# Optimization experiments

Measured on AMD Instinct MI355X. Metric: run time of the kernel, lower is better.

The kernel has to match this reference:

```python
import jax, jax.numpy as jnp
import numpy as np

N = 100000
E = 1600000
IN, HID, OUT = 512, 256, 32
K = 3
LAMBDA_AMP = 0.5


def setup_inputs() -> dict:
    key = jax.random.key(0)
    ks = jax.random.split(key, 6)
    x = jax.random.normal(ks[0], (N, IN), dtype=jnp.float32)
    edge_index = jax.random.randint(ks[1], (2, E), 0, N, dtype=jnp.int64)
    # MLP params (PyTorch Linear default init: U(-1/sqrt(fan_in), 1/sqrt(fan_in)))
    s1 = 1.0 / np.sqrt(IN)
    W1 = jax.random.uniform(ks[2], (IN, HID), jnp.float32, -s1, s1)
    b1 = jax.random.uniform(ks[3], (HID,), jnp.float32, -s1, s1)
    s2 = 1.0 / np.sqrt(HID)
    W2 = jax.random.uniform(ks[4], (HID, OUT), jnp.float32, -s2, s2)
    b2 = jax.random.uniform(ks[5], (OUT,), jnp.float32, -s2, s2)
    return {"x": x, "W1": W1, "b1": b1, "W2": W2, "b2": b2, "edge_index": edge_index}


def _gcn_norm(edge_index, n_nodes, dtype):
    # add self loops, symmetric normalization D^-1/2 (A+I) D^-1/2
    loop = jnp.arange(n_nodes, dtype=edge_index.dtype)
    row = jnp.concatenate([edge_index[0], loop])
    col = jnp.concatenate([edge_index[1], loop])
    w = jnp.ones(row.shape[0], dtype=dtype)
    deg = jax.ops.segment_sum(w, col, num_segments=n_nodes)
    dis = jnp.where(deg > 0, jax.lax.rsqrt(deg), 0.0)
    norm = dis[row] * w * dis[col]
    return row, col, norm


def _proximal_l21(x, lam):
    # row-wise soft-thresholding of L2 norms
    rn = jnp.sqrt(jnp.sum(x * x, axis=1))  # [N]
    safe = jnp.where(rn > 0, rn, 1.0)
    score = jnp.where(rn > 0, jnp.maximum(rn - lam, 0.0) / safe, 0.0)
    return score[:, None] * x


def reference(x, W1, b1, W2, b2, edge_index):
    # MLP (dropout inactive at inference)
    h = jax.nn.relu(x @ W1 + b1)
    h = h @ W2 + b2  # [N, OUT]

    row, col, norm = _gcn_norm(edge_index, N, h.dtype)

    lam = LAMBDA_AMP
    gamma = 1.0 / (2.0 * (1.0 - lam))
    hh = h
    xk = h
    for _ in range(K):
        # A_hat @ xk via gather-scale-scatter
        ax = jax.ops.segment_sum(norm[:, None] * xk[row], col, num_segments=N)
        lx = xk - ax  # L @ xk
        y = xk - gamma * 2.0 * (1.0 - lam) * lx
        xk = hh + _proximal_l21(y - hh, lam * gamma)
    return xk
```

## Files before the change

### kernel.cpp

```cpp
#include <hip/hip_runtime.h>
#include <cstdint>

#define NN 100000
#define EE 1600000
#define IN_F 512
#define HID_F 256
#define OUT_F 32
#define GSL 256
#define SLICE_W 12500
#define CAP 64

typedef float f32x4 __attribute__((ext_vector_type(4)));
typedef int   i32x4 __attribute__((ext_vector_type(4)));
typedef short s16x8 __attribute__((ext_vector_type(8)));
typedef uint32_t u32x4 __attribute__((ext_vector_type(4)));
typedef unsigned short u16;

static __device__ __forceinline__ u16 f2bf(float f) {
  uint32_t u = __builtin_bit_cast(uint32_t, f);
  u += 0x7FFFu + ((u >> 16) & 1u);
  return (u16)(u >> 16);
}

static __device__ __forceinline__ float bf2f(u16 v) {
  uint32_t u = ((uint32_t)v) << 16;
  return __builtin_bit_cast(float, u);
}

static __device__ __forceinline__ uint32_t pk_bf16(float a, float b) {
  uint32_t r;
  asm("v_cvt_pk_bf16_f32 %0, %1, %2" : "=v"(r) : "v"(a), "v"(b));
  return r;
}

__global__ __launch_bounds__(256) void k_prep(const float* __restrict__ w1,
                                              u16* __restrict__ w1f,
                                              const float* __restrict__ w2,
                                              u16* __restrict__ w2f,
                                              int* __restrict__ cur) {
  int b = blockIdx.x;
  int tid = threadIdx.x;
  if (b < 512) {
    int g = b * 256 + tid;
    int j    = g & 7;
    int lane = (g >> 3) & 63;
    int fnG  = (g >> 9) & 15;
    int kk   = g >> 13;
    int k = kk * 32 + (lane >> 4) * 8 + j;
    int n = fnG * 16 + (lane & 15);
    w1f[g] = f2bf(w1[k * HID_F + n]);
  } else if (b < 544) {
    int g = (b - 512) * 256 + tid;
    int j    = g & 7;
    int lane = (g >> 3) & 63;
    int ff   = g >> 9;
    int k = (ff >> 1) * 32 + (lane >> 4) * 8 + j;
    int n = (ff & 1) * 16 + (lane & 15);
    w2f[g] = f2bf(w2[k * OUT_F + n]);
  } else {
    int i = (b - 544) * 256 + tid;
    if (i < NN) cur[i] = 0;
  }
}

__global__ __launch_bounds__(256) void k_fillC(const int* __restrict__ row,
                                               const int* __restrict__ col,
                                               int* __restrict__ cur,
                                               int* __restrict__ csr) {
  const int slice = blockIdx.x & 7;
  const int g = blockIdx.x >> 3;
  const unsigned lo = (unsigned)slice * SLICE_W, hi = lo + SLICE_W;
  const i32x4* c4 = (const i32x4*)col;
  const i32x4* r4 = (const i32x4*)row;
  for (int i = g * 256 + threadIdx.x; i < EE / 4; i += GSL * 256) {
    i32x4 c = c4[i];
    i32x4 r = r4[i];
    #pragma unroll
    for (int k = 0; k < 4; ++k) {
      unsigned cc = (unsigned)c[k];
      if (cc >= lo && cc < hi) {
        int p = atomicAdd(&cur[cc], 1);
        if (p < CAP) csr[(int)cc * CAP + p] = r[k];
      }
    }
  }
}

__global__ __launch_bounds__(256, 4) void k_mlp(
    const float* __restrict__ x, const float* __restrict__ b1,
    const float* __restrict__ b2, const u16* __restrict__ w1f,
    const u16* __restrict__ w2f, const int* __restrict__ cnt,
    float* __restrict__ hout, u16* __restrict__ xs0) {
  __shared__ char smem[32768];
  char* aL  = smem;
  char* h1L = smem;

  const int tid  = threadIdx.x;
  const int lane = tid & 63;
  const int wid  = tid >> 6;
  const int wn   = wid;
  const int l16  = lane & 15;
  const int lq   = lane >> 4;
  const int row0 = blockIdx.x * 64;

  const f32x4 zf = {0.f, 0.f, 0.f, 0.f};
  f32x4 acc[4][4];
  #pragma unroll
  for (int i = 0; i < 4; ++i)
    #pragma unroll
    for (int j = 0; j < 4; ++j) acc[i][j] = zf;

  for (int kt = 0; kt < IN_F / 64; ++kt) {
    __syncthreads();
    #pragma unroll
    for (int p = 0; p < 4; ++p) {
      int v   = p * 256 + tid;
      int row = v >> 4;
      int f4  = v & 15;
      int grow = row0 + row;
      f32x4 xv = zf;
      if (grow < NN)
        xv = *(const f32x4*)(x + (size_t)grow * IN_F + kt * 64 + f4 * 4);
      uint32_t lo = pk_bf16(xv.x, xv.y);
      uint32_t hi = pk_bf16(xv.z, xv.w);
      uint64_t wv = (uint64_t)lo | ((uint64_t)hi << 32);
      int kb = (f4 * 8) ^ ((row & 7) << 4);
      *(uint64_t*)(aL + row * 128 + kb) = wv;
    }
    __syncthreads();
    #pragma unroll
    for (int ks = 0; ks < 2; ++ks) {
      const int kk = kt * 2 + ks;
      s16x8 af[4], bf[4];
      #pragma unroll
      for (int fn = 0; fn < 4; ++fn)
        bf[fn] = *(const s16x8*)(w1f + ((size_t)(kk * 16 + wn * 4 + fn) * 64 + lane) * 8);
      #pragma unroll
      for (int fm = 0; fm < 4; ++fm) {
        int row = fm * 16 + l16;
        int kb  = (ks * 64 + lq * 16) ^ ((row & 7) << 4);
        af[fm] = *(const s16x8*)(aL + row * 128 + kb);
      }
      #pragma unroll
      for (int fm = 0; fm < 4; ++fm)
        #pragma unroll
        for (int fn = 0; fn < 4; ++fn)
          acc[fm][fn] = __builtin_amdgcn_mfma_f32_16x16x32_bf16(
              af[fm], bf[fn], acc[fm][fn], 0, 0, 0);
    }
  }

  float b1v[4];
  #pragma unroll
  for (int fn = 0; fn < 4; ++fn) b1v[fn] = b1[wn * 64 + fn * 16 + l16];

  __syncthreads();
  #pragma unroll
  for (int fm = 0; fm < 4; ++fm) {
    #pragma unroll
    for (int fn = 0; fn < 4; ++fn) {
      int col = wn * 64 + fn * 16 + l16;
      #pragma unroll
      for (int r = 0; r < 4; ++r) {
        int row = fm * 16 + lq * 4 + r;
        float v = acc[fm][fn][r] + b1v[fn];
        v = fmaxf(v, 0.f);
        *(u16*)(h1L + row * 512 + ((col * 2) ^ ((row & 7) << 4))) = f2bf(v);
      }
    }
  }
  __syncthreads();

  f32x4 acc2[2];
  acc2[0] = zf; acc2[1] = zf;
  const int arow = wid * 16 + l16;
  #pragma unroll
  for (int ks = 0; ks < 8; ++ks) {
    int kb = ks * 64 + lq * 16;
    s16x8 af = *(const s16x8*)(h1L + arow * 512 + (kb ^ ((arow & 7) << 4)));
    #pragma unroll
    for (int fn = 0; fn < 2; ++fn) {
      s16x8 bfr = *(const s16x8*)(w2f + ((size_t)((ks * 2 + fn) * 64) + lane) * 8);
      acc2[fn] = __builtin_amdgcn_mfma_f32_16x16x32_bf16(af, bfr, acc2[fn], 0, 0, 0);
    }
  }
  #pragma unroll
  for (int r = 0; r < 4; ++r) {
    int row = row0 + wid * 16 + lq * 4 + r;
    if (row >= NN) continue;
    float dr = rsqrtf((float)cnt[row] + 1.0f);
    #pragma unroll
    for (int fn = 0; fn < 2; ++fn) {
      int col = fn * 16 + l16;
      float v = acc2[fn][r] + b2[col];
      hout[(size_t)row * 32 + col] = v;
      xs0[(size_t)row * 32 + col] = f2bf(dr * v);
    }
  }
}

template <int LAST>
__global__ __launch_bounds__(256) void k_prop(
    const u16* __restrict__ xs, const float* __restrict__ hh,
    u16* __restrict__ xs_out, float* __restrict__ fout,
    const int* __restrict__ cnt, const int* __restrict__ csr) {
  int w = blockIdx.x * 4 + (threadIdx.x >> 6);
  if (w >= NN) return;
  const int lane = threadIdx.x & 63;
  const int q = lane & 3;
  const int s = lane >> 2;
  const int n = cnt[w];
  const int* __restrict__ crow = csr + (size_t)w * CAP;
  float acc[8] = {0.f, 0.f, 0.f, 0.f, 0.f, 0.f, 0.f, 0.f};
  for (int j = s; j < n; j += 16) {
    int src = crow[j];
    s16x8 v = *(const s16x8*)(xs + (size_t)src * 32 + q * 8);
    #pragma unroll
    for (int k = 0; k < 8; ++k) acc[k] += bf2f((u16)v[k]);
  }
  if (s == 0) {
    s16x8 v = *(const s16x8*)(xs + (size_t)w * 32 + q * 8);
    #pragma unroll
    for (int k = 0; k < 8; ++k) acc[k] += bf2f((u16)v[k]);
  }
  #pragma unroll
  for (int m = 4; m <= 32; m <<= 1) {
    #pragma unroll
    for (int k = 0; k < 8; ++k) acc[k] += __shfl_xor(acc[k], m, 64);
  }
  const float di = rsqrtf((float)n + 1.0f);
  const f32x4 h0 = *(const f32x4*)(hh + (size_t)w * 32 + q * 8);
  const f32x4 h1 = *(const f32x4*)(hh + (size_t)w * 32 + q * 8 + 4);
  float hv[8] = {h0.x, h0.y, h0.z, h0.w, h1.x, h1.y, h1.z, h1.w};
  float d[8];
  float rn2 = 0.f;
  #pragma unroll
  for (int k = 0; k < 8; ++k) {
    d[k] = di * acc[k] - hv[k];
    rn2 += d[k] * d[k];
  }
  rn2 += __shfl_xor(rn2, 1, 64);
  rn2 += __shfl_xor(rn2, 2, 64);
  float rn = sqrtf(rn2);
  float sc = (rn > 0.f) ? fmaxf(rn - 0.5f, 0.f) / rn : 0.f;
  if (s == 0) {
    if (LAST) {
      f32x4 o0, o1;
      o0.x = hv[0] + sc * d[0]; o0.y = hv[1] + sc * d[1];
      o0.z = hv[2] + sc * d[2]; o0.w = hv[3] + sc * d[3];
      o1.x = hv[4] + sc * d[4]; o1.y = hv[5] + sc * d[5];
      o1.z = hv[6] + sc * d[6]; o1.w = hv[7] + sc * d[7];
      *(f32x4*)(fout + (size_t)w * 32 + q * 8) = o0;
      *(f32x4*)(fout + (size_t)w * 32 + q * 8 + 4) = o1;
    } else {
      s16x8 o;
      #pragma unroll
      for (int k = 0; k < 8; ++k) o[k] = (short)f2bf(di * (hv[k] + sc * d[k]));
      *(s16x8*)(xs_out + (size_t)w * 32 + q * 8) = o;
    }
  }
}

extern "C" void kernel_launch(void* const* d_in, const int* in_sizes, int n_in,
                              void* d_out, int out_size, void* d_ws, size_t ws_size,
                              hipStream_t stream) {
  const float* x  = (const float*)d_in[0];
  const float* W1 = (const float*)d_in[1];
  const float* b1 = (const float*)d_in[2];
  const float* W2 = (const float*)d_in[3];
  const float* b2 = (const float*)d_in[4];
  const int*   ei = (const int*)d_in[5];

  char* ws = (char*)d_ws;
  float* h    = (float*)(ws);
  u16*   xs0  = (u16*)  (ws + 12800000);
  u16*   xs1  = (u16*)  (ws + 19200000);
  int*   csr  = (int*)  (ws + 25600000);
  int*   cur  = (int*)  (ws + 51200000);
  u16*   w1f  = (u16*)  (ws + 51600000);
  u16*   w2f  = (u16*)  (ws + 51862144);

  k_prep<<<935, 256, 0, stream>>>(W1, w1f, W2, w2f, cur);
  k_fillC<<<8 * GSL, 256, 0, stream>>>(ei, ei + EE, cur, csr);
  k_mlp<<<(NN + 63) / 64, 256, 0, stream>>>(x, b1, b2, w1f, w2f, cur, h, xs0);

  float* out = (float*)d_out;
  k_prop<0><<<(NN + 3) / 4, 256, 0, stream>>>(xs0, h, xs1, nullptr, cur, csr);
  k_prop<0><<<(NN + 3) / 4, 256, 0, stream>>>(xs1, h, xs0, nullptr, cur, csr);
  k_prop<1><<<(NN + 3) / 4, 256, 0, stream>>>(xs0, h, nullptr, out,  cur, csr);
}
```

Before: 276.7 us.

## Double-buffer MLP input tile with register prefetch and 128-row blocks

The MLP kernel now handles 128 rows per block with 512 threads arranged as a 2x4 wave grid. It ping-pongs between two LDS buffers, loading the next 64-column slice of x into registers while the MFMAs run on the current slice. The aim is to hide global-load latency of the large fp32 input and to reuse each W1 fragment across more rows. In exchange the block uses 64KB of shared memory and more registers, which limits how many blocks fit per CU.

```diff
diff --git a/kernel.cpp b/kernel.cpp
--- a/kernel.cpp
+++ b/kernel.cpp
@@ -86,48 +86,69 @@
   }
 }
 
-__global__ __launch_bounds__(256, 4) void k_mlp(
+__global__ __launch_bounds__(512) void k_mlp(
     const float* __restrict__ x, const float* __restrict__ b1,
     const float* __restrict__ b2, const u16* __restrict__ w1f,
     const u16* __restrict__ w2f, const int* __restrict__ cnt,
     float* __restrict__ hout, u16* __restrict__ xs0) {
-  __shared__ char smem[32768];
-  char* aL  = smem;
+  __shared__ char smem[65536];
+  char* aL0 = smem;
+  char* aL1 = smem + 16384;
   char* h1L = smem;
 
   const int tid  = threadIdx.x;
   const int lane = tid & 63;
   const int wid  = tid >> 6;
-  const int wn   = wid;
+  const int wm   = wid >> 2;
+  const int wn   = wid & 3;
   const int l16  = lane & 15;
   const int lq   = lane >> 4;
-  const int row0 = blockIdx.x * 64;
+  const int row0 = blockIdx.x * 128;
 
   const f32x4 zf = {0.f, 0.f, 0.f, 0.f};
-  f32x4 acc[4][4];
-  #pragma unroll
-  for (int i = 0; i < 4; ++i)
-    #pragma unroll
-    for (int j = 0; j < 4; ++j) acc[i][j] = zf;
-
-  for (int kt = 0; kt < IN_F / 64; ++kt) {
-    __syncthreads();
+
+  auto loadA = [&](int kt, f32x4 ar[4]) {
     #pragma unroll
     for (int p = 0; p < 4; ++p) {
-      int v   = p * 256 + tid;
+      int v   = p * 512 + tid;
       int row = v >> 4;
       int f4  = v & 15;
       int grow = row0 + row;
-      f32x4 xv = zf;
+      ar[p] = zf;
       if (grow < NN)
-        xv = *(const f32x4*)(x + (size_t)grow * IN_F + kt * 64 + f4 * 4);
-      uint32_t lo = pk_bf16(xv.x, xv.y);
-      uint32_t hi = pk_bf16(xv.z, xv.w);
+        ar[p] = *(const f32x4*)(x + (size_t)grow * IN_F + kt * 64 + f4 * 4);
+    }
+  };
+  auto writeA = [&](char* buf, f32x4 ar[4]) {
+    #pragma unroll
+    for (int p = 0; p < 4; ++p) {
+      int v   = p * 512 + tid;
+      int row = v >> 4;
+      int f4  = v & 15;
+      uint32_t lo = pk_bf16(ar[p].x, ar[p].y);
+      uint32_t hi = pk_bf16(ar[p].z, ar[p].w);
       uint64_t wv = (uint64_t)lo | ((uint64_t)hi << 32);
       int kb = (f4 * 8) ^ ((row & 7) << 4);
-      *(uint64_t*)(aL + row * 128 + kb) = wv;
-    }
+      *(uint64_t*)(buf + row * 128 + kb) = wv;
+    }
+  };
+
+  f32x4 acc[4][4];
+  #pragma unroll
+  for (int i = 0; i < 4; ++i)
+    #pragma unroll
+    for (int j = 0; j < 4; ++j) acc[i][j] = zf;
+
+  f32x4 ar[4];
+  loadA(0, ar);
+  writeA(aL0, ar);
+
+  #pragma unroll
+  for (int kt = 0; kt < IN_F / 64; ++kt) {
+    char* aCur = (kt & 1) ? aL1 : aL0;
+    char* aNxt = (kt & 1) ? aL0 : aL1;
     __syncthreads();
+    if (kt < 7) loadA(kt + 1, ar);
     #pragma unroll
     for (int ks = 0; ks < 2; ++ks) {
       const int kk = kt * 2 + ks;
@@ -137,9 +158,9 @@
         bf[fn] = *(const s16x8*)(w1f + ((size_t)(kk * 16 + wn * 4 + fn) * 64 + lane) * 8);
       #pragma unroll
       for (int fm = 0; fm < 4; ++fm) {
-        int row = fm * 16 + l16;
+        int row = wm * 64 + fm * 16 + l16;
         int kb  = (ks * 64 + lq * 16) ^ ((row & 7) << 4);
-        af[fm] = *(const s16x8*)(aL + row * 128 + kb);
+        af[fm] = *(const s16x8*)(aCur + row * 128 + kb);
       }
       #pragma unroll
       for (int fm = 0; fm < 4; ++fm)
@@ -148,6 +169,7 @@
           acc[fm][fn] = __builtin_amdgcn_mfma_f32_16x16x32_bf16(
               af[fm], bf[fn], acc[fm][fn], 0, 0, 0);
     }
+    if (kt < 7) writeA(aNxt, ar);
   }
 
   float b1v[4];
@@ -162,7 +184,7 @@
       int col = wn * 64 + fn * 16 + l16;
       #pragma unroll
       for (int r = 0; r < 4; ++r) {
-        int row = fm * 16 + lq * 4 + r;
+        int row = wm * 64 + fm * 16 + lq * 4 + r;
         float v = acc[fm][fn][r] + b1v[fn];
         v = fmaxf(v, 0.f);
         *(u16*)(h1L + row * 512 + ((col * 2) ^ ((row & 7) << 4))) = f2bf(v);
@@ -282,7 +304,7 @@
 
   k_prep<<<935, 256, 0, stream>>>(W1, w1f, W2, w2f, cur);
   k_fillC<<<8 * GSL, 256, 0, stream>>>(ei, ei + EE, cur, csr);
-  k_mlp<<<(NN + 63) / 64, 256, 0, stream>>>(x, b1, b2, w1f, w2f, cur, h, xs0);
+  k_mlp<<<(NN + 127) / 128, 512, 0, stream>>>(x, b1, b2, w1f, w2f, cur, h, xs0);
 
   float* out = (float*)d_out;
   k_prop<0><<<(NN + 3) / 4, 256, 0, stream>>>(xs0, h, xs1, nullptr, cur, csr);
```

Result: slower. 284.2 us (+2.7%).
